# Kernel optimization log

Measured on AMD Instinct MI355X. Metric: run time of the kernel, lower is better.

The kernel has to match this reference:

```python
import jax, jax.numpy as jnp
import numpy as np

B, N, E = 2, 50000, 400000
FIN, HID, OUT = 128, 128, 128
EPS = 1e-5  # BatchNorm1d default eps


def setup_inputs() -> dict:
    key = jax.random.key(0)
    ks = jax.random.split(key, 12)
    x = jax.random.normal(ks[0], (B, N, FIN), dtype=jnp.float32)
    row = jax.random.randint(ks[1], (E,), 0, N, dtype=jnp.int32)          # scatter dst
    col = jnp.concatenate([jnp.arange(N, dtype=jnp.int32),                # ensure deg>=1
                           jax.random.randint(ks[2], (E - N,), 0, N, dtype=jnp.int32)])
    edge_index = jnp.stack([row, col])                                    # [2, E]
    deg = jnp.zeros((N,), jnp.float32).at[col].add(1.0)                   # degree(col, N)
    dis = deg ** -0.5
    norm = (dis[row] * dis[col])[None, :, None]                           # [1, E, 1]
    W1 = jax.random.normal(ks[3], (HID, FIN), jnp.float32) / np.sqrt(FIN)
    b1 = jax.random.normal(ks[4], (HID,), jnp.float32) * 0.01
    g1 = jnp.ones((N,), jnp.float32)
    be1 = jnp.zeros((N,), jnp.float32)
    W2 = jax.random.normal(ks[5], (OUT, HID), jnp.float32) / np.sqrt(HID)
    b2 = jax.random.normal(ks[6], (OUT,), jnp.float32) * 0.01
    g2 = jnp.ones((N,), jnp.float32)
    be2 = jnp.zeros((N,), jnp.float32)
    return {"x": x, "edge_index": edge_index, "norm": norm,
            "W1": W1, "b1": b1, "g1": g1, "be1": be1,
            "W2": W2, "b2": b2, "g2": g2, "be2": be2}


def _gcn_layer(x, edge_index, norm, W, b, g, be):
    # Linear (dropout p=0 -> identity)
    h = jnp.einsum('bnf,of->bno', x, W) + b                 # [B, N, C]
    # BatchNorm1d(num_features=N): per-node stats over (batch, channel)
    mu = jnp.mean(h, axis=(0, 2), keepdims=True)            # [1, N, 1]
    var = jnp.var(h, axis=(0, 2), keepdims=True)            # biased, as torch
    y = g[None, :, None] * (h - mu) * jax.lax.rsqrt(var + EPS) + be[None, :, None]
    a = jax.nn.gelu(y, approximate=False)                   # torch GELU = exact erf
    # message passing: gather src nodes, scale by norm, scatter-add to dst
    msgs = a[:, edge_index[1], :] * norm                    # [B, E, C]
    return jnp.zeros_like(a).at[:, edge_index[0], :].add(msgs)


def reference(x, edge_index, norm, W1, b1, g1, be1, W2, b2, g2, be2):
    x = _gcn_layer(x, edge_index, norm, W1, b1, g1, be1)
    x = _gcn_layer(x, edge_index, norm, W2, b2, g2, be2)
    return x
```

## Files before the change

kernel.cpp:

```cpp
#include <hip/hip_runtime.h>
#include <math.h>

#define CC 128

typedef unsigned short u16;
typedef short bf16x8 __attribute__((ext_vector_type(8)));
typedef float f32x4 __attribute__((ext_vector_type(4)));

typedef __attribute__((address_space(3))) void lds_t;
typedef const __attribute__((address_space(1))) void gbl_t;

__device__ __forceinline__ u16 f2bf(float f) {
    union { float f; unsigned u; } v; v.f = f;
    unsigned u = v.u;
    return (u16)((u + 0x7FFFu + ((u >> 16) & 1u)) >> 16);
}
__device__ __forceinline__ float bf2f(unsigned hi16) {
    union { unsigned u; float f; } v; v.u = hi16 << 16; return v.f;
}
__device__ __forceinline__ unsigned cvt_pk(float lo, float hi) {
    unsigned r;
    asm("v_cvt_pk_bf16_f32 %0, %1, %2" : "=v"(r) : "v"(lo), "v"(hi));
    return r;
}

__device__ __forceinline__ float gelu_f(float y) {
    float xa = fabsf(y) * 0.70710678118654752f;
    float t  = __builtin_amdgcn_rcpf(fmaf(0.3275911f, xa, 1.0f));
    float p  = fmaf(1.061405429f, t, -1.453152027f);
    p = fmaf(p, t, 1.421413741f);
    p = fmaf(p, t, -0.284496736f);
    p = fmaf(p, t, 0.254829592f);
    p *= t;
    float e  = __expf(-xa * xa);
    float er = fmaf(-p, e, 1.0f);
    float s  = copysignf(er, y);
    return 0.5f * y * (1.0f + s);
}


__global__ __launch_bounds__(256) void k_zero_i32(int* __restrict__ p, int n) {
    int i = blockIdx.x * 256 + threadIdx.x;
    if (i < n) p[i] = 0;
}

__global__ __launch_bounds__(256) void k_hist(const int* __restrict__ row, int* __restrict__ cnt, int E) {
    int e = blockIdx.x * 256 + threadIdx.x;
    if (e < E) atomicAdd(&cnt[row[e]], 1);
}

__device__ __forceinline__ int wave_incl_scan(int v) {
    #pragma unroll
    for (int d = 1; d < 64; d <<= 1) {
        int t = __shfl_up(v, d);
        if ((threadIdx.x & 63) >= d) v += t;
    }
    return v;
}

__global__ __launch_bounds__(256) void k_scan_a(const int* __restrict__ cnt, int* __restrict__ bsum, int N) {
    int base = blockIdx.x * 1024 + threadIdx.x * 4;
    int s = 0;
    #pragma unroll
    for (int u = 0; u < 4; ++u) { int i = base + u; if (i < N) s += cnt[i]; }
    #pragma unroll
    for (int d = 32; d > 0; d >>= 1) s += __shfl_down(s, d);
    __shared__ int wsum[4];
    if ((threadIdx.x & 63) == 0) wsum[threadIdx.x >> 6] = s;
    __syncthreads();
    if (threadIdx.x == 0) bsum[blockIdx.x] = wsum[0] + wsum[1] + wsum[2] + wsum[3];
}

__global__ __launch_bounds__(64) void k_scan_b(const int* __restrict__ bsum, int* __restrict__ boff,
                                               int* __restrict__ off, int N, int nb) {
    int carry = 0;
    for (int base = 0; base < nb; base += 64) {
        int t = base + (int)threadIdx.x;
        int v = (t < nb) ? bsum[t] : 0;
        int incl = wave_incl_scan(v);
        if (t < nb) boff[t] = carry + incl - v;
        carry += __shfl(incl, 63);
    }
    if (threadIdx.x == 0) off[N] = carry;
}

__global__ __launch_bounds__(256) void k_scan_c(int* __restrict__ cnt, const int* __restrict__ boff,
                                                int* __restrict__ off, int N) {
    int t = threadIdx.x;
    int base = blockIdx.x * 1024 + t * 4;
    int v[4]; int s = 0;
    #pragma unroll
    for (int u = 0; u < 4; ++u) { int i = base + u; v[u] = (i < N) ? cnt[i] : 0; s += v[u]; }
    int incl = wave_incl_scan(s);
    __shared__ int wsum[4];
    int w = t >> 6, lane = t & 63;
    if (lane == 63) wsum[w] = incl;
    __syncthreads();
    int run = incl - s + boff[blockIdx.x];
    for (int ww = 0; ww < w; ++ww) run += wsum[ww];
    #pragma unroll
    for (int u = 0; u < 4; ++u) {
        int i = base + u;
        if (i < N) { off[i] = run; cnt[i] = 0; }
        run += v[u];
    }
}

__global__ __launch_bounds__(256) void k_fill(const int* __restrict__ row, const int* __restrict__ col,
                                              const float* __restrict__ nrm, const int* __restrict__ off,
                                              int* __restrict__ cur, int2* __restrict__ eg, int E) {
    int e = blockIdx.x * 256 + threadIdx.x;
    if (e < E) {
        int r = row[e];
        int p = off[r] + atomicAdd(&cur[r], 1);
        eg[p] = make_int2(col[e], __float_as_int(nrm[e]));
    }
}

__global__ __launch_bounds__(256) void k_wrepack(const float* __restrict__ W1, u16* __restrict__ Wp1,
                                                 const float* __restrict__ W2, u16* __restrict__ Wp2) {
    int i = blockIdx.x * 256 + threadIdx.x;
    if (i < 2 * CC * CC) {
        int is2 = (i >= CC * CC);
        int ii = is2 ? i - CC * CC : i;
        int j = ii & 7, l = (ii >> 3) & 63, s = (ii >> 9) & 3, t = ii >> 11;
        int r = 16 * t + (l & 15);
        int p = s * 32 + ((l >> 4) & 3) * 8 + j;
        if (is2) {
            int k = (p & 7) * 16 + (p >> 3);
            Wp2[ii] = f2bf(W2[r * CC + k]);
        } else {
            Wp1[ii] = f2bf(W1[r * CC + p]);
        }
    }
}

__global__ __launch_bounds__(256) void k_fused_l1(
    const float* __restrict__ X, const u16* __restrict__ Wp1, const u16* __restrict__ Wp2,
    const float* __restrict__ bias, const float* __restrict__ gamma, const float* __restrict__ beta,
    u16* __restrict__ Z, int N)
{
    __shared__ __align__(16) u16 WS[CC * CC];
    __shared__ __align__(16) unsigned TT[4][16][68];

    const int tid = threadIdx.x;
    const int w = tid >> 6;
    const int l = tid & 63;
    const int g = l >> 4;
    const int c = l & 15;
    const int n8 = blockIdx.x * 32 + w * 8;
    const bool valid = n8 < N;
    const int nbase = valid ? n8 : 0;

    #pragma unroll
    for (int it = 0; it < 8; ++it) {
        const u16* gsrc = Wp1 + it * 2048 + w * 512 + l * 8;
        u16* ldst = &WS[it * 2048 + w * 512];
        __builtin_amdgcn_global_load_lds((gbl_t*)gsrc, (lds_t*)ldst, 16, 0, 0);
    }

    const int ab = c >> 3;
    const int an = nbase + (c & 7);
    const float* xbase = X + ((size_t)ab * N + an) * CC + g * 8;
    bf16x8 af[4];
    #pragma unroll
    for (int s = 0; s < 4; ++s) {
        float4 lo = *(const float4*)(xbase + s * 32);
        float4 hi = *(const float4*)(xbase + s * 32 + 4);
        unsigned aw[4];
        aw[0] = cvt_pk(lo.x, lo.y); aw[1] = cvt_pk(lo.z, lo.w);
        aw[2] = cvt_pk(hi.x, hi.y); aw[3] = cvt_pk(hi.z, hi.w);
        af[s] = *(bf16x8*)aw;
    }

    float bb[8];
    #pragma unroll
    for (int t = 0; t < 8; ++t) bb[t] = bias[t * 16 + c];
    float gam[4], bet[4];
    #pragma unroll
    for (int r = 0; r < 4; ++r) {
        int p = (4 * g + r) & 7;
        gam[r] = gamma[nbase + p];
        bet[r] = beta[nbase + p];
    }

    __syncthreads();

    f32x4 acc[8];
    #pragma unroll
    for (int t = 0; t < 8; ++t) acc[t] = (f32x4){0.f, 0.f, 0.f, 0.f};
    #pragma unroll
    for (int s = 0; s < 4; ++s) {
        bf16x8 bf[8];
        #pragma unroll
        for (int t = 0; t < 8; ++t)
            bf[t] = *(const bf16x8*)&WS[((t * 4 + s) * 64 + l) * 8];
        #pragma unroll
        for (int t = 0; t < 8; ++t)
            acc[t] = __builtin_amdgcn_mfma_f32_16x16x32_bf16(af[s], bf[t], acc[t], 0, 0, 0);
    }

    __syncthreads();

    #pragma unroll
    for (int it = 0; it < 8; ++it) {
        const u16* gsrc = Wp2 + it * 2048 + w * 512 + l * 8;
        u16* ldst = &WS[it * 2048 + w * 512];
        __builtin_amdgcn_global_load_lds((gbl_t*)gsrc, (lds_t*)ldst, 16, 0, 0);
    }

    float rs[4] = {0.f, 0.f, 0.f, 0.f}, rq[4] = {0.f, 0.f, 0.f, 0.f};
    #pragma unroll
    for (int t = 0; t < 8; ++t)
        #pragma unroll
        for (int r = 0; r < 4; ++r) {
            float h = acc[t][r] + bb[t];
            acc[t][r] = h;
            rs[r] += h;
            rq[r] += h * h;
        }
    #pragma unroll
    for (int d = 1; d < 16; d <<= 1) {
        #pragma unroll
        for (int r = 0; r < 4; ++r) {
            rs[r] += __shfl_xor(rs[r], d);
            rq[r] += __shfl_xor(rq[r], d);
        }
    }
    #pragma unroll
    for (int r = 0; r < 4; ++r) {
        rs[r] += __shfl_xor(rs[r], 32);
        rq[r] += __shfl_xor(rq[r], 32);
    }

    #pragma unroll
    for (int r = 0; r < 4; ++r) {
        float mean = rs[r] * (1.f / 256.f);
        float var  = rq[r] * (1.f / 256.f) - mean * mean;
        float sc = gam[r] * rsqrtf(fmaxf(var, 0.f) + 1e-5f);
        float sh = bet[r] - mean * sc;
        #pragma unroll
        for (int t = 0; t < 8; ++t)
            acc[t][r] = gelu_f(acc[t][r] * sc + sh);
    }

    #pragma unroll
    for (int r = 0; r < 4; ++r) {
        unsigned tw[4];
        #pragma unroll
        for (int tt = 0; tt < 4; ++tt)
            tw[tt] = cvt_pk(acc[2 * tt][r], acc[2 * tt + 1][r]);
        *(uint4*)&TT[w][4 * g + r][c * 4] = *(uint4*)tw;
    }
    bf16x8 af2[4];
    #pragma unroll
    for (int s = 0; s < 4; ++s)
        af2[s] = *(const bf16x8*)&TT[w][c][s * 16 + g * 4];

    __syncthreads();

    f32x4 acc2[8];
    #pragma unroll
    for (int t = 0; t < 8; ++t) acc2[t] = (f32x4){0.f, 0.f, 0.f, 0.f};
    #pragma unroll
    for (int s = 0; s < 4; ++s) {
        bf16x8 bf[8];
        #pragma unroll
        for (int t = 0; t < 8; ++t)
            bf[t] = *(const bf16x8*)&WS[((t * 4 + s) * 64 + l) * 8];
        #pragma unroll
        for (int t = 0; t < 8; ++t)
            acc2[t] = __builtin_amdgcn_mfma_f32_16x16x32_bf16(af2[s], bf[t], acc2[t], 0, 0, 0);
    }

    if (valid) {
        #pragma unroll
        for (int r = 0; r < 4; ++r) {
            int rr = 4 * g + r;
            int db = rr >> 3, dn = n8 + (rr & 7);
            unsigned zw[4];
            #pragma unroll
            for (int tt = 0; tt < 4; ++tt)
                zw[tt] = cvt_pk(acc2[2 * tt][r], acc2[2 * tt + 1][r]);
            *(uint4*)(Z + ((size_t)dn * 2 + db) * CC + c * 8) = *(uint4*)zw;
        }
    }
}

__global__ __launch_bounds__(256) void k_agg_bn(
    const u16* __restrict__ Zin, const int* __restrict__ off, const int2* __restrict__ eg,
    const float* __restrict__ b2, const float* __restrict__ g2, const float* __restrict__ be2,
    u16* __restrict__ A2, int N, int nw)
{
    __shared__ u16 TW[4][256];
    const int wv = threadIdx.x >> 6;
    const int l = threadIdx.x & 63;
    const int p = l >> 5;
    const int b = (l >> 4) & 1;
    const int c = l & 15;
    const u16* Ab = Zin + b * CC + c * 8;
    float bb[8];
    #pragma unroll
    for (int t = 0; t < 8; ++t) bb[t] = b2[t * 16 + c];

    for (int n = blockIdx.x * 4 + wv; n < N; n += nw) {
        int s = off[n], e = off[n + 1];
        float a[8] = {0.f, 0.f, 0.f, 0.f, 0.f, 0.f, 0.f, 0.f};
        for (int j = s; j < e; j += 8) {
            int base = j + 4 * p;
            uint4 ea = *(const uint4*)&eg[base];
            uint4 eb = *(const uint4*)&eg[base + 2];
            int s0 = (base     < e) ? (int)ea.x : 0; float w0 = (base     < e) ? __int_as_float((int)ea.y) : 0.f;
            int s1 = (base + 1 < e) ? (int)ea.z : 0; float w1 = (base + 1 < e) ? __int_as_float((int)ea.w) : 0.f;
            int s2 = (base + 2 < e) ? (int)eb.x : 0; float w2 = (base + 2 < e) ? __int_as_float((int)eb.y) : 0.f;
            int s3 = (base + 3 < e) ? (int)eb.z : 0; float w3 = (base + 3 < e) ? __int_as_float((int)eb.w) : 0.f;
            bf16x8 v0 = *(const bf16x8*)(Ab + (size_t)s0 * 256);
            bf16x8 v1 = *(const bf16x8*)(Ab + (size_t)s1 * 256);
            bf16x8 v2 = *(const bf16x8*)(Ab + (size_t)s2 * 256);
            bf16x8 v3 = *(const bf16x8*)(Ab + (size_t)s3 * 256);
            #pragma unroll
            for (int q = 0; q < 8; ++q) {
                a[q] = fmaf(w0, bf2f((u16)v0[q]), a[q]);
                a[q] = fmaf(w1, bf2f((u16)v1[q]), a[q]);
                a[q] = fmaf(w2, bf2f((u16)v2[q]), a[q]);
                a[q] = fmaf(w3, bf2f((u16)v3[q]), a[q]);
            }
        }
        #pragma unroll
        for (int q = 0; q < 8; ++q) a[q] += __shfl_xor(a[q], 32);

        float ss = 0.f, qq = 0.f;
        #pragma unroll
        for (int t = 0; t < 8; ++t) {
            float h = a[t] + bb[t];
            a[t] = h;
            ss += h;
            qq += h * h;
        }
        #pragma unroll
        for (int d = 1; d < 32; d <<= 1) {
            ss += __shfl_xor(ss, d);
            qq += __shfl_xor(qq, d);
        }
        float mean = ss * (1.f / 256.f);
        float var  = qq * (1.f / 256.f) - mean * mean;
        float sc = g2[n] * rsqrtf(fmaxf(var, 0.f) + 1e-5f);
        float sh = be2[n] - mean * sc;

        #pragma unroll
        for (int u = 0; u < 4; ++u) {
            int q = 4 * p + u;
            TW[wv][b * CC + q * 16 + c] = f2bf(gelu_f(a[q] * sc + sh));
        }
        uint2 v = *(const uint2*)&TW[wv][l * 4];
        *(uint2*)(A2 + (size_t)n * 256 + l * 4) = v;
    }
}

__global__ __launch_bounds__(256) void k_agg_out(
    const u16* __restrict__ A2, const int* __restrict__ off, const int2* __restrict__ eg,
    float* __restrict__ Out, int N, int nw)
{
    const int l = threadIdx.x & 63;
    const int p = l >> 5;
    const int sl = l & 31;
    const u16* Ab = A2 + sl * 8;

    for (int n = blockIdx.x * 4 + (threadIdx.x >> 6); n < N; n += nw) {
        int s = off[n], e = off[n + 1];
        float a[8] = {0.f, 0.f, 0.f, 0.f, 0.f, 0.f, 0.f, 0.f};
        for (int j = s; j < e; j += 8) {
            int base = j + 4 * p;
            uint4 ea = *(const uint4*)&eg[base];
            uint4 eb = *(const uint4*)&eg[base + 2];
            int s0 = (base     < e) ? (int)ea.x : 0; float w0 = (base     < e) ? __int_as_float((int)ea.y) : 0.f;
            int s1 = (base + 1 < e) ? (int)ea.z : 0; float w1 = (base + 1 < e) ? __int_as_float((int)ea.w) : 0.f;
            int s2 = (base + 2 < e) ? (int)eb.x : 0; float w2 = (base + 2 < e) ? __int_as_float((int)eb.y) : 0.f;
            int s3 = (base + 3 < e) ? (int)eb.z : 0; float w3 = (base + 3 < e) ? __int_as_float((int)eb.w) : 0.f;
            bf16x8 v0 = *(const bf16x8*)(Ab + (size_t)s0 * 256);
            bf16x8 v1 = *(const bf16x8*)(Ab + (size_t)s1 * 256);
            bf16x8 v2 = *(const bf16x8*)(Ab + (size_t)s2 * 256);
            bf16x8 v3 = *(const bf16x8*)(Ab + (size_t)s3 * 256);
            #pragma unroll
            for (int q = 0; q < 8; ++q) {
                a[q] = fmaf(w0, bf2f((u16)v0[q]), a[q]);
                a[q] = fmaf(w1, bf2f((u16)v1[q]), a[q]);
                a[q] = fmaf(w2, bf2f((u16)v2[q]), a[q]);
                a[q] = fmaf(w3, bf2f((u16)v3[q]), a[q]);
            }
        }
        #pragma unroll
        for (int q = 0; q < 8; ++q) a[q] += __shfl_xor(a[q], 32);

        int bb_ = sl >> 4;
        int ch0 = (sl & 15) * 8;
        float* d = Out + ((size_t)bb_ * N + n) * CC + ch0 + 4 * p;
        *(float4*)d = make_float4(a[4 * p + 0], a[4 * p + 1], a[4 * p + 2], a[4 * p + 3]);
    }
}


extern "C" void kernel_launch(void* const* d_in, const int* in_sizes, int n_in,
                              void* d_out, int out_size, void* d_ws, size_t ws_size,
                              hipStream_t stream)
{
    const float* x   = (const float*)d_in[0];
    const int*   ei  = (const int*)d_in[1];
    const float* nrm = (const float*)d_in[2];
    const float* W1  = (const float*)d_in[3];
    const float* b1  = (const float*)d_in[4];
    const float* g1  = (const float*)d_in[5];
    const float* be1 = (const float*)d_in[6];
    const float* W2  = (const float*)d_in[7];
    const float* b2  = (const float*)d_in[8];
    const float* g2  = (const float*)d_in[9];
    const float* be2 = (const float*)d_in[10];

    const int N = in_sizes[5];
    const int E = in_sizes[2];
    const int* row = ei;
    const int* col = ei + E;
    const int nb = (N + 1023) / 1024;

    auto al = [](size_t v) { return (v + 255) & ~(size_t)255; };
    char* p = (char*)d_ws;
    int* off    = (int*)p;   p += al((size_t)(N + 1) * 4);
    int* cur    = (int*)p;   p += al((size_t)N * 4);
    int2* eg    = (int2*)p;  p += al((size_t)(E + 8) * 8);
    int* bsum   = (int*)p;   p += al((size_t)nb * 4);
    int* boff   = (int*)p;   p += al((size_t)nb * 4);
    u16* Wp1    = (u16*)p;   p += al((size_t)CC * CC * 2);
    u16* Wp2    = (u16*)p;   p += al((size_t)CC * CC * 2);
    u16* Zbuf   = (u16*)p;   p += al((size_t)2 * N * CC * 2);
    u16* A2buf  = (u16*)p;   p += al((size_t)2 * N * CC * 2);

    k_zero_i32<<<(N + 255) / 256, 256, 0, stream>>>(cur, N);
    k_hist<<<(E + 255) / 256, 256, 0, stream>>>(row, cur, E);
    k_scan_a<<<nb, 256, 0, stream>>>(cur, bsum, N);
    k_scan_b<<<1, 64, 0, stream>>>(bsum, boff, off, N, nb);
    k_scan_c<<<nb, 256, 0, stream>>>(cur, boff, off, N);
    k_fill<<<(E + 255) / 256, 256, 0, stream>>>(row, col, nrm, off, cur, eg, E);

    k_wrepack<<<(2 * CC * CC + 255) / 256, 256, 0, stream>>>(W1, Wp1, W2, Wp2);

    const int gb = (N + 31) / 32;
    const int AGG_BLOCKS = 2048;
    const int nwaves = AGG_BLOCKS * 4;
    k_fused_l1<<<gb, 256, 0, stream>>>(x, Wp1, Wp2, b1, g1, be1, Zbuf, N);
    k_agg_bn<<<AGG_BLOCKS, 256, 0, stream>>>(Zbuf, off, eg, b2, g2, be2, A2buf, N, nwaves);
    k_agg_out<<<AGG_BLOCKS, 256, 0, stream>>>(A2buf, off, eg, (float*)d_out, N, nwaves);
}
```

Baseline: 165.6 us.

## Map one node per half-wave in aggregation kernels, drop grid-stride loop

Both aggregation kernels now give each 32-lane half-wave its own destination node. Previously a full wave handled one node, with its two halves splitting the edges and then combining partials by shuffle. The persistent grid-stride loop is replaced with one node per half-wave over a grid sized to N. This removes the cross-half shuffle reduction and doubles the number of nodes in flight per wave, at the cost of divergence between halves when node degrees differ. The edge loads change from 16-byte vector loads to separate int2 loads.

New measurement: 153.2 us. -7.5%, faster.

```diff
diff --git a/kernel.cpp b/kernel.cpp
--- a/kernel.cpp
+++ b/kernel.cpp
@@ -290,112 +290,113 @@
 __global__ __launch_bounds__(256) void k_agg_bn(
     const u16* __restrict__ Zin, const int* __restrict__ off, const int2* __restrict__ eg,
     const float* __restrict__ b2, const float* __restrict__ g2, const float* __restrict__ be2,
-    u16* __restrict__ A2, int N, int nw)
+    u16* __restrict__ A2, int N)
 {
-    __shared__ u16 TW[4][256];
+    __shared__ u16 TW[4][2][256];
     const int wv = threadIdx.x >> 6;
     const int l = threadIdx.x & 63;
-    const int p = l >> 5;
-    const int b = (l >> 4) & 1;
-    const int c = l & 15;
+    const int half = l >> 5;
+    const int h = l & 31;
+    const int b = h >> 4;
+    const int c = h & 15;
+    const int n = blockIdx.x * 8 + wv * 2 + half;
+    const bool nv = n < N;
+    const int nn = nv ? n : 0;
     const u16* Ab = Zin + b * CC + c * 8;
+
     float bb[8];
     #pragma unroll
     for (int t = 0; t < 8; ++t) bb[t] = b2[t * 16 + c];
 
-    for (int n = blockIdx.x * 4 + wv; n < N; n += nw) {
-        int s = off[n], e = off[n + 1];
-        float a[8] = {0.f, 0.f, 0.f, 0.f, 0.f, 0.f, 0.f, 0.f};
-        for (int j = s; j < e; j += 8) {
-            int base = j + 4 * p;
-            uint4 ea = *(const uint4*)&eg[base];
-            uint4 eb = *(const uint4*)&eg[base + 2];
-            int s0 = (base     < e) ? (int)ea.x : 0; float w0 = (base     < e) ? __int_as_float((int)ea.y) : 0.f;
-            int s1 = (base + 1 < e) ? (int)ea.z : 0; float w1 = (base + 1 < e) ? __int_as_float((int)ea.w) : 0.f;
-            int s2 = (base + 2 < e) ? (int)eb.x : 0; float w2 = (base + 2 < e) ? __int_as_float((int)eb.y) : 0.f;
-            int s3 = (base + 3 < e) ? (int)eb.z : 0; float w3 = (base + 3 < e) ? __int_as_float((int)eb.w) : 0.f;
-            bf16x8 v0 = *(const bf16x8*)(Ab + (size_t)s0 * 256);
-            bf16x8 v1 = *(const bf16x8*)(Ab + (size_t)s1 * 256);
-            bf16x8 v2 = *(const bf16x8*)(Ab + (size_t)s2 * 256);
-            bf16x8 v3 = *(const bf16x8*)(Ab + (size_t)s3 * 256);
-            #pragma unroll
-            for (int q = 0; q < 8; ++q) {
-                a[q] = fmaf(w0, bf2f((u16)v0[q]), a[q]);
-                a[q] = fmaf(w1, bf2f((u16)v1[q]), a[q]);
-                a[q] = fmaf(w2, bf2f((u16)v2[q]), a[q]);
-                a[q] = fmaf(w3, bf2f((u16)v3[q]), a[q]);
-            }
-        }
-        #pragma unroll
-        for (int q = 0; q < 8; ++q) a[q] += __shfl_xor(a[q], 32);
-
-        float ss = 0.f, qq = 0.f;
-        #pragma unroll
-        for (int t = 0; t < 8; ++t) {
-            float h = a[t] + bb[t];
-            a[t] = h;
-            ss += h;
-            qq += h * h;
-        }
-        #pragma unroll
-        for (int d = 1; d < 32; d <<= 1) {
-            ss += __shfl_xor(ss, d);
-            qq += __shfl_xor(qq, d);
-        }
-        float mean = ss * (1.f / 256.f);
-        float var  = qq * (1.f / 256.f) - mean * mean;
-        float sc = g2[n] * rsqrtf(fmaxf(var, 0.f) + 1e-5f);
-        float sh = be2[n] - mean * sc;
-
-        #pragma unroll
-        for (int u = 0; u < 4; ++u) {
-            int q = 4 * p + u;
-            TW[wv][b * CC + q * 16 + c] = f2bf(gelu_f(a[q] * sc + sh));
-        }
-        uint2 v = *(const uint2*)&TW[wv][l * 4];
-        *(uint2*)(A2 + (size_t)n * 256 + l * 4) = v;
+    int s = off[nn];
+    int e = nv ? off[nn + 1] : 0;
+    float a[8] = {0.f, 0.f, 0.f, 0.f, 0.f, 0.f, 0.f, 0.f};
+    for (int j = s; j < e; j += 4) {
+        int2 e0 = eg[j], e1 = eg[j + 1], e2 = eg[j + 2], e3 = eg[j + 3];
+        int s0 = e0.x;                  float w0 = __int_as_float(e0.y);
+        int s1 = (j + 1 < e) ? e1.x : 0; float w1 = (j + 1 < e) ? __int_as_float(e1.y) : 0.f;
+        int s2 = (j + 2 < e) ? e2.x : 0; float w2 = (j + 2 < e) ? __int_as_float(e2.y) : 0.f;
+        int s3 = (j + 3 < e) ? e3.x : 0; float w3 = (j + 3 < e) ? __int_as_float(e3.y) : 0.f;
+        bf16x8 v0 = *(const bf16x8*)(Ab + (size_t)s0 * 256);
+        bf16x8 v1 = *(const bf16x8*)(Ab + (size_t)s1 * 256);
+        bf16x8 v2 = *(const bf16x8*)(Ab + (size_t)s2 * 256);
+        bf16x8 v3 = *(const bf16x8*)(Ab + (size_t)s3 * 256);
+        #pragma unroll
+        for (int q = 0; q < 8; ++q) {
+            a[q] = fmaf(w0, bf2f((u16)v0[q]), a[q]);
+            a[q] = fmaf(w1, bf2f((u16)v1[q]), a[q]);
+            a[q] = fmaf(w2, bf2f((u16)v2[q]), a[q]);
+            a[q] = fmaf(w3, bf2f((u16)v3[q]), a[q]);
+        }
+    }
+
+    float ss = 0.f, qq = 0.f;
+    #pragma unroll
+    for (int t = 0; t < 8; ++t) {
+        float hh = a[t] + bb[t];
+        a[t] = hh;
+        ss += hh;
+        qq += hh * hh;
+    }
+    #pragma unroll
+    for (int d = 1; d < 32; d <<= 1) {
+        ss += __shfl_xor(ss, d);
+        qq += __shfl_xor(qq, d);
+    }
+    float mean = ss * (1.f / 256.f);
+    float var  = qq * (1.f / 256.f) - mean * mean;
+    float sc = g2[nn] * rsqrtf(fmaxf(var, 0.f) + 1e-5f);
+    float sh = be2[nn] - mean * sc;
+
+    #pragma unroll
+    for (int t = 0; t < 8; ++t)
+        TW[wv][half][b * CC + t * 16 + c] = f2bf(gelu_f(a[t] * sc + sh));
+    if (nv) {
+        bf16x8 v = *(const bf16x8*)&TW[wv][half][h * 8];
+        *(bf16x8*)(A2 + (size_t)nn * 256 + h * 8) = v;
     }
 }
 
 __global__ __launch_bounds__(256) void k_agg_out(
     const u16* __restrict__ A2, const int* __restrict__ off, const int2* __restrict__ eg,
-    float* __restrict__ Out, int N, int nw)
+    float* __restrict__ Out, int N)
 {
+    const int wv = threadIdx.x >> 6;
     const int l = threadIdx.x & 63;
-    const int p = l >> 5;
-    const int sl = l & 31;
-    const u16* Ab = A2 + sl * 8;
-
-    for (int n = blockIdx.x * 4 + (threadIdx.x >> 6); n < N; n += nw) {
-        int s = off[n], e = off[n + 1];
-        float a[8] = {0.f, 0.f, 0.f, 0.f, 0.f, 0.f, 0.f, 0.f};
-        for (int j = s; j < e; j += 8) {
-            int base = j + 4 * p;
-            uint4 ea = *(const uint4*)&eg[base];
-            uint4 eb = *(const uint4*)&eg[base + 2];
-            int s0 = (base     < e) ? (int)ea.x : 0; float w0 = (base     < e) ? __int_as_float((int)ea.y) : 0.f;
-            int s1 = (base + 1 < e) ? (int)ea.z : 0; float w1 = (base + 1 < e) ? __int_as_float((int)ea.w) : 0.f;
-            int s2 = (base + 2 < e) ? (int)eb.x : 0; float w2 = (base + 2 < e) ? __int_as_float((int)eb.y) : 0.f;
-            int s3 = (base + 3 < e) ? (int)eb.z : 0; float w3 = (base + 3 < e) ? __int_as_float((int)eb.w) : 0.f;
-            bf16x8 v0 = *(const bf16x8*)(Ab + (size_t)s0 * 256);
-            bf16x8 v1 = *(const bf16x8*)(Ab + (size_t)s1 * 256);
-            bf16x8 v2 = *(const bf16x8*)(Ab + (size_t)s2 * 256);
-            bf16x8 v3 = *(const bf16x8*)(Ab + (size_t)s3 * 256);
-            #pragma unroll
-            for (int q = 0; q < 8; ++q) {
-                a[q] = fmaf(w0, bf2f((u16)v0[q]), a[q]);
-                a[q] = fmaf(w1, bf2f((u16)v1[q]), a[q]);
-                a[q] = fmaf(w2, bf2f((u16)v2[q]), a[q]);
-                a[q] = fmaf(w3, bf2f((u16)v3[q]), a[q]);
-            }
-        }
-        #pragma unroll
-        for (int q = 0; q < 8; ++q) a[q] += __shfl_xor(a[q], 32);
-
-        int bb_ = sl >> 4;
-        int ch0 = (sl & 15) * 8;
-        float* d = Out + ((size_t)bb_ * N + n) * CC + ch0 + 4 * p;
-        *(float4*)d = make_float4(a[4 * p + 0], a[4 * p + 1], a[4 * p + 2], a[4 * p + 3]);
+    const int half = l >> 5;
+    const int h = l & 31;
+    const int b = h >> 4;
+    const int c = h & 15;
+    const int n = blockIdx.x * 8 + wv * 2 + half;
+    const bool nv = n < N;
+    const int nn = nv ? n : 0;
+    const u16* Ab = A2 + h * 8;
+
+    int s = off[nn];
+    int e = nv ? off[nn + 1] : 0;
+    float a[8] = {0.f, 0.f, 0.f, 0.f, 0.f, 0.f, 0.f, 0.f};
+    for (int j = s; j < e; j += 4) {
+        int2 e0 = eg[j], e1 = eg[j + 1], e2 = eg[j + 2], e3 = eg[j + 3];
+        int s0 = e0.x;                  float w0 = __int_as_float(e0.y);
+        int s1 = (j + 1 < e) ? e1.x : 0; float w1 = (j + 1 < e) ? __int_as_float(e1.y) : 0.f;
+        int s2 = (j + 2 < e) ? e2.x : 0; float w2 = (j + 2 < e) ? __int_as_float(e2.y) : 0.f;
+        int s3 = (j + 3 < e) ? e3.x : 0; float w3 = (j + 3 < e) ? __int_as_float(e3.y) : 0.f;
+        bf16x8 v0 = *(const bf16x8*)(Ab + (size_t)s0 * 256);
+        bf16x8 v1 = *(const bf16x8*)(Ab + (size_t)s1 * 256);
+        bf16x8 v2 = *(const bf16x8*)(Ab + (size_t)s2 * 256);
+        bf16x8 v3 = *(const bf16x8*)(Ab + (size_t)s3 * 256);
+        #pragma unroll
+        for (int q = 0; q < 8; ++q) {
+            a[q] = fmaf(w0, bf2f((u16)v0[q]), a[q]);
+            a[q] = fmaf(w1, bf2f((u16)v1[q]), a[q]);
+            a[q] = fmaf(w2, bf2f((u16)v2[q]), a[q]);
+            a[q] = fmaf(w3, bf2f((u16)v3[q]), a[q]);
+        }
+    }
+    if (nv) {
+        float* d = Out + ((size_t)b * N + nn) * CC + c * 8;
+        *(float4*)&d[0] = make_float4(a[0], a[1], a[2], a[3]);
+        *(float4*)&d[4] = make_float4(a[4], a[5], a[6], a[7]);
     }
 }
 
@@ -444,9 +445,8 @@
     k_wrepack<<<(2 * CC * CC + 255) / 256, 256, 0, stream>>>(W1, Wp1, W2, Wp2);
 
     const int gb = (N + 31) / 32;
-    const int AGG_BLOCKS = 2048;
-    const int nwaves = AGG_BLOCKS * 4;
+    const int ga = (N + 7) / 8;
     k_fused_l1<<<gb, 256, 0, stream>>>(x, Wp1, Wp2, b1, g1, be1, Zbuf, N);
-    k_agg_bn<<<AGG_BLOCKS, 256, 0, stream>>>(Zbuf, off, eg, b2, g2, be2, A2buf, N, nwaves);
-    k_agg_out<<<AGG_BLOCKS, 256, 0, stream>>>(A2buf, off, eg, (float*)d_out, N, nwaves);
-}
+    k_agg_bn<<<ga, 256, 0, stream>>>(Zbuf, off, eg, b2, g2, be2, A2buf, N);
+    k_agg_out<<<ga, 256, 0, stream>>>(A2buf, off, eg, (float*)d_out, N);
+}
```
